# Kernel optimization log

Hardware: AMD Instinct MI355X
Metric: run time of the kernel (lower is better)

## Reference

```python
import jax, jax.numpy as jnp
import numpy as np

EPS_NORM = 1e-12  # torch F.normalize eps
EPS_POOL = 1e-06
GAMMA = 10.0
TOPK = 32


def _l2norm(x, axis):
    n = jnp.sqrt(jnp.sum(x * x, axis=axis, keepdims=True))
    return x / jnp.maximum(n, EPS_NORM)


def _sae(x, enc, dec_w, dec_b):
    # x: [N, D]; enc: [H, D]; dec_w: [D, H]; dec_b: [D]
    w = _l2norm(enc, axis=1)
    x_n = _l2norm(x, axis=-1)
    cos = jnp.clip(x_n @ w.T, -1.0, 1.0)           # [N, H]
    acts = 2.0 - jnp.sqrt(2.0 - 2.0 * cos)
    vals, idx = jax.lax.top_k(acts, TOPK)           # [N, K]
    rows = jnp.arange(acts.shape[0])[:, None]
    sparse = jnp.zeros_like(acts).at[rows, idx].set(vals)
    recon = sparse @ dec_w.T + dec_b                # [N, D]
    return recon, sparse


def _sample_views(v_pad, centers, H, W):
    # v_pad: [B, Lmax, D], centers: [B, K, 2]; uniform grid HxW per batch
    L = H * W
    y = (jnp.arange(H, dtype=jnp.float32) + 0.5) / H
    x = (jnp.arange(W, dtype=jnp.float32) + 0.5) / W
    gy, gx = jnp.meshgrid(y, x, indexing='ij')
    coords = jnp.stack([gx.ravel(), gy.ravel()], axis=-1)        # [L, 2] (x, y)
    diff = centers[:, :, None, :] - coords[None, None, :, :]     # [B, K, L, 2]
    m = jnp.exp(-GAMMA * jnp.sum(diff * diff, axis=-1))          # [B, K, L]
    num = jnp.einsum('bkl,bld->bkd', m, v_pad[:, :L, :])
    den = jnp.sum(m, axis=-1, keepdims=True) + EPS_POOL
    return num / den                                             # [B, K, D]


def setup_inputs() -> dict:
    key = jax.random.key(0)
    ks = jax.random.split(key, 10)
    B, Lmax, D, Hh, T, K = 64, 1024, 1024, 16384, 512, 8
    fan_in = D
    bound = 1.0 / np.sqrt(fan_in)
    return {
        'v_pad': jax.random.normal(ks[0], (B, Lmax, D), jnp.float32),
        'v_len': jnp.full((B,), Lmax, dtype=jnp.int32),
        'grid_thws': jnp.tile(jnp.array([[1, 32, 32]], dtype=jnp.int32), (B, 1)),
        't_pad': jax.random.normal(ks[1], (B, T, D), jnp.float32),
        't_mask': jnp.ones((B, T), jnp.float32),
        'centers': jax.random.uniform(ks[2], (B, K, 2), jnp.float32),
        'enc_v': jax.random.normal(ks[3], (Hh, D), jnp.float32) * 0.02,
        'dec_v_w': jax.random.uniform(ks[4], (D, Hh), jnp.float32, -bound, bound),
        'dec_v_b': jnp.zeros((D,), jnp.float32),
        'enc_t': jax.random.normal(ks[5], (Hh, D), jnp.float32) * 0.02,
        'dec_t_w': jax.random.uniform(ks[6], (D, Hh), jnp.float32, -bound, bound),
        'dec_t_b': jnp.zeros((D,), jnp.float32),
    }


def reference(v_pad, v_len, grid_thws, t_pad, t_mask, centers,
              enc_v, dec_v_w, dec_v_b, enc_t, dec_t_w, dec_t_b):
    H = int(np.asarray(grid_thws)[0, 1])
    W = int(np.asarray(grid_thws)[0, 2])
    # text global pooling
    t_sum = jnp.sum(t_pad * t_mask[..., None], axis=1)
    t_global = t_sum / (jnp.sum(t_mask, axis=1, keepdims=True) + EPS_POOL)
    # gaussian view pooling
    v_views = _sample_views(v_pad, centers, H, W)                 # [B, K, D]
    recon_t, latent_t = _sae(t_global, enc_t, dec_t_w, dec_t_b)
    B, K, D = v_views.shape
    recon_v_flat, latent_v_flat = _sae(v_views.reshape(B * K, D), enc_v, dec_v_w, dec_v_b)
    recon_v = recon_v_flat.reshape(B, K, D)
    latent_v = latent_v_flat.reshape(B, K, -1)
    return (recon_v, v_views, recon_t, t_global, latent_v, latent_t)
```

## Files before the change

### kernel.cpp

```cpp
#include <hip/hip_runtime.h>
#include <hip/hip_bf16.h>

constexpr int NB    = 64;
constexpr int LMAX  = 1024;
constexpr int DD    = 1024;
constexpr int HSAE  = 16384;
constexpr int TT    = 512;
constexpr int KV    = 8;
constexpr int TOPK  = 32;
constexpr int NROW_V = NB * KV;
constexpr int NROW_T = NB;

constexpr size_t OUT_RECON_V = 0;
constexpr size_t OUT_VVIEWS  = OUT_RECON_V + (size_t)NROW_V * DD;
constexpr size_t OUT_RECON_T = OUT_VVIEWS + (size_t)NROW_V * DD;
constexpr size_t OUT_TGLOBAL = OUT_RECON_T + (size_t)NROW_T * DD;
constexpr size_t OUT_LAT_V   = OUT_TGLOBAL + (size_t)NROW_T * DD;
constexpr size_t OUT_LAT_T   = OUT_LAT_V + (size_t)NROW_V * HSAE;

constexpr size_t WS_VN     = 0;
constexpr size_t WS_TN     = WS_VN + (size_t)NROW_V * DD;
constexpr size_t WS_IDX_V  = WS_TN + (size_t)NROW_T * DD;
constexpr size_t WS_VAL_V  = WS_IDX_V + (size_t)NROW_V * TOPK;
constexpr size_t WS_IDX_T  = WS_VAL_V + (size_t)NROW_V * TOPK;
constexpr size_t WS_VAL_T  = WS_IDX_T + (size_t)NROW_T * TOPK;
constexpr size_t WS_BINV_V = WS_VAL_T + (size_t)NROW_T * TOPK;
constexpr size_t WS_BINV_T = WS_BINV_V + (size_t)HSAE;
constexpr size_t WS_AHI_V  = WS_BINV_T + (size_t)HSAE;
constexpr size_t WS_AHI_T  = WS_AHI_V + (size_t)NROW_V * DD / 2;

constexpr int LC  = 8;
constexpr int LCH = LMAX / LC;
constexpr int TC  = 8;
constexpr int TCH = TT / TC;
constexpr size_t PV_NUM = 0;
constexpr size_t PV_DEN = (size_t)NB * LC * KV * DD;
constexpr size_t PT_NUM = 0;
constexpr size_t PT_DEN = (size_t)NB * TC * DD;

typedef __attribute__((ext_vector_type(8))) short bf16x8;
typedef __attribute__((ext_vector_type(4))) short s16x4;
typedef __attribute__((ext_vector_type(4))) float f32x4;

__device__ inline unsigned short f2bf_rn(float x) {
    unsigned u = __float_as_uint(x);
    return (unsigned short)((u + 0x7FFFu + ((u >> 16) & 1u)) >> 16);
}
__device__ inline double shfl_down_dbl(double x, int off) {
    long long l = __double_as_longlong(x);
    int lo = (int)(l & 0xffffffffll), hi = (int)(l >> 32);
    lo = __shfl_down(lo, off); hi = __shfl_down(hi, off);
    return __longlong_as_double(((long long)hi << 32) | (unsigned long long)(unsigned int)lo);
}

__global__ __launch_bounds__(256) void pool_part_kernel(const float* __restrict__ v_pad,
                                                        const float* __restrict__ centers,
                                                        const int* __restrict__ grid_thws,
                                                        const float* __restrict__ t_pad,
                                                        const float* __restrict__ t_mask,
                                                        float* __restrict__ partV,
                                                        float* __restrict__ partT) {
    __shared__ float m_s[LCH * KV];
    const int b   = blockIdx.x;
    const int tid = threadIdx.x;

    if (blockIdx.y < LC) {
        const int lc = blockIdx.y;
        const int H = grid_thws[1];
        const int W = grid_thws[2];
        int L = H * W; if (L > LMAX) L = LMAX;
        const int l0 = lc * LCH;

        for (int i = tid; i < LCH * KV; i += 256) {
            const int ll = i >> 3, k = i & 7;
            const int l  = l0 + ll;
            float m = 0.f;
            if (l < L) {
                const int iy = l / W, ix = l - iy * W;
                const float gx = (ix + 0.5f) / (float)W;
                const float gy = (iy + 0.5f) / (float)H;
                const float dx = centers[((size_t)b * KV + k) * 2 + 0] - gx;
                const float dy = centers[((size_t)b * KV + k) * 2 + 1] - gy;
                m = expf(-10.f * (dx * dx + dy * dy));
            }
            m_s[ll * KV + k] = m;
        }
        __syncthreads();
        if (tid < KV) {
            float s = 0.f;
            for (int ll = 0; ll < LCH; ++ll) s += m_s[ll * KV + tid];
            partV[PV_DEN + ((size_t)b * LC + lc) * KV + tid] = s;
        }

        const float* vp = v_pad + ((size_t)b * LMAX + l0) * DD + tid * 4;
        float4 acc[KV];
#pragma unroll
        for (int k = 0; k < KV; ++k) acc[k] = make_float4(0.f, 0.f, 0.f, 0.f);
#pragma unroll 4
        for (int ll = 0; ll < LCH; ++ll) {
            const float4 v = *(const float4*)(vp + (size_t)ll * DD);
#pragma unroll
            for (int k = 0; k < KV; ++k) {
                const float m = m_s[ll * KV + k];
                acc[k].x = fmaf(m, v.x, acc[k].x); acc[k].y = fmaf(m, v.y, acc[k].y);
                acc[k].z = fmaf(m, v.z, acc[k].z); acc[k].w = fmaf(m, v.w, acc[k].w);
            }
        }
#pragma unroll
        for (int k = 0; k < KV; ++k)
            *(float4*)(partV + PV_NUM + (((size_t)b * LC + lc) * KV + k) * DD + tid * 4) = acc[k];
    } else {
        const int tc = blockIdx.y - LC;
        const int t0 = tc * TCH;
        if (tid < TCH) m_s[tid] = t_mask[(size_t)b * TT + t0 + tid];
        __syncthreads();
        if (tid == 0) {
            float s = 0.f;
            for (int i = 0; i < TCH; ++i) s += m_s[i];
            partT[PT_DEN + (size_t)b * TC + tc] = s;
        }
        const float* tp = t_pad + ((size_t)b * TT + t0) * DD + tid * 4;
        float4 acc = make_float4(0.f, 0.f, 0.f, 0.f);
#pragma unroll 4
        for (int t = 0; t < TCH; ++t) {
            const float4 v = *(const float4*)(tp + (size_t)t * DD);
            const float m = m_s[t];
            acc.x = fmaf(m, v.x, acc.x); acc.y = fmaf(m, v.y, acc.y);
            acc.z = fmaf(m, v.z, acc.z); acc.w = fmaf(m, v.w, acc.w);
        }
        *(float4*)(partT + PT_NUM + ((size_t)b * TC + tc) * DD + tid * 4) = acc;
    }
}

__device__ inline void comb_norm_emit(float4 vv, int r, int tid,
                                      float* __restrict__ out_row,
                                      float* __restrict__ ws, size_t xn_off, size_t hi_off) {
    *(float4*)(out_row + tid * 4) = vv;
    float ss = vv.x * vv.x + vv.y * vv.y + vv.z * vv.z + vv.w * vv.w;
#pragma unroll
    for (int off = 32; off; off >>= 1) ss += __shfl_down(ss, off);
    __shared__ float wsum[4];
    if ((tid & 63) == 0) wsum[tid >> 6] = ss;
    __syncthreads();
    const float tot = wsum[0] + wsum[1] + wsum[2] + wsum[3];
    const float scale = 1.f / fmaxf(sqrtf(tot), 1e-12f);
    float4 xn;
    xn.x = vv.x * scale; xn.y = vv.y * scale; xn.z = vv.z * scale; xn.w = vv.w * scale;
    *(float4*)(ws + xn_off + (size_t)r * DD + tid * 4) = xn;
    const float f[4] = {xn.x, xn.y, xn.z, xn.w};
    s16x4 hv;
#pragma unroll
    for (int c = 0; c < 4; ++c) hv[c] = (short)f2bf_rn(f[c]);
    *(s16x4*)((short*)(ws + hi_off) + (size_t)r * DD + tid * 4) = hv;
}

__global__ __launch_bounds__(256) void pool_comb_kernel(const float* __restrict__ partV,
                                                        const float* __restrict__ partT,
                                                        float* __restrict__ out_views,
                                                        float* __restrict__ out_tg,
                                                        float* __restrict__ ws) {
    const int b   = blockIdx.x;
    const int k   = blockIdx.y;
    const int tid = threadIdx.x;
    if (k < KV) {
        float den = 1e-6f;
        for (int lc = 0; lc < LC; ++lc) den += partV[PV_DEN + ((size_t)b * LC + lc) * KV + k];
        float4 s = make_float4(0.f, 0.f, 0.f, 0.f);
        for (int lc = 0; lc < LC; ++lc) {
            const float4 p = *(const float4*)(partV + PV_NUM + (((size_t)b * LC + lc) * KV + k) * DD + tid * 4);
            s.x += p.x; s.y += p.y; s.z += p.z; s.w += p.w;
        }
        const float inv = 1.f / den;
        float4 vv = make_float4(s.x * inv, s.y * inv, s.z * inv, s.w * inv);
        const int r = b * KV + k;
        comb_norm_emit(vv, r, tid, out_views + (size_t)r * DD, ws, WS_VN, WS_AHI_V);
    } else {
        float den = 1e-6f;
        for (int tc = 0; tc < TC; ++tc) den += partT[PT_DEN + (size_t)b * TC + tc];
        float4 s = make_float4(0.f, 0.f, 0.f, 0.f);
        for (int tc = 0; tc < TC; ++tc) {
            const float4 p = *(const float4*)(partT + PT_NUM + ((size_t)b * TC + tc) * DD + tid * 4);
            s.x += p.x; s.y += p.y; s.z += p.z; s.w += p.w;
        }
        const float inv = 1.f / den;
        float4 vv = make_float4(s.x * inv, s.y * inv, s.z * inv, s.w * inv);
        comb_norm_emit(vv, b, tid, out_tg + (size_t)b * DD, ws, WS_TN, WS_AHI_T);
    }
}

constexpr int GBM = 128, GBN = 64, GBK = 32;

__device__ inline int fragoff(int sub, int g, int r16) {
    return (((sub * 4 + g) * 16) + (r16 ^ ((g & 3) << 1))) * 8;
}

__global__ __launch_bounds__(256) void gemm_acts_mfma(const float* __restrict__ encV,
                                                      const float* __restrict__ encT,
                                                      float* __restrict__ out,
                                                      float* __restrict__ ws) {
    __shared__ short Ah[GBM * GBK];
    __shared__ short Bh[GBN * GBK], Bl[GBN * GBK];
    __shared__ float bn_part[GBN][4];
    __shared__ float binv_s[GBN];

    const int tid  = threadIdx.x;
    const int lane = tid & 63;
    const int wv   = tid >> 6;
    const int wm   = wv & 1;
    const int wn   = wv >> 1;
    const int bid  = blockIdx.x;
    const int xcd  = bid & 7;
    const int slot = bid >> 3;
    const int hb   = xcd + 8 * (slot / 5);
    const int my   = slot % 5;
    const bool isT = (my == 4);
    const int h0   = hb * GBN;
    const int m0   = isT ? 0 : my * GBM;
    const int M    = isT ? NROW_T : NROW_V;
    const float* Bm = isT ? encT : encV;
    const short* AhiP = (const short*)(ws + (isT ? WS_AHI_T : WS_AHI_V));
    float* outActs = out + (isT ? OUT_LAT_T : OUT_LAT_V);
    float* binv_g  = ws + (isT ? WS_BINV_T : WS_BINV_V);

    const int ksS = tid & 3;
    int lrA[2];
#pragma unroll
    for (int rt = 0; rt < 2; ++rt) lrA[rt] = (rt * 256 + tid) >> 2;
    const int lrB = tid >> 2;

    f32x4 acc[4][2];
#pragma unroll
    for (int mi = 0; mi < 4; ++mi)
#pragma unroll
        for (int ni = 0; ni < 2; ++ni) acc[mi][ni] = (f32x4){0.f, 0.f, 0.f, 0.f};
    float bnacc = 0.f;

    bf16x8 pa[2];
    float4 pb0, pb1;

    auto issue_loads = [&](int kt) {
#pragma unroll
        for (int rt = 0; rt < 2; ++rt) {
            if (m0 + lrA[rt] < M)
                pa[rt] = *(const bf16x8*)&AhiP[(size_t)(m0 + lrA[rt]) * DD + kt + ksS * 8];
            else
                pa[rt] = (bf16x8){0, 0, 0, 0, 0, 0, 0, 0};
        }
        const float* src = Bm + (size_t)(h0 + lrB) * DD + kt + ksS * 8;
        pb0 = *(const float4*)src;
        pb1 = *(const float4*)(src + 4);
    };

    auto write_lds = [&]() {
#pragma unroll
        for (int rt = 0; rt < 2; ++rt)
            *(bf16x8*)&Ah[fragoff(lrA[rt] >> 4, ksS, lrA[rt] & 15)] = pa[rt];
        {
            const float f[8] = {pb0.x, pb0.y, pb0.z, pb0.w, pb1.x, pb1.y, pb1.z, pb1.w};
            bf16x8 hv, lv;
            float bsum = 0.f;
#pragma unroll
            for (int j = 0; j < 8; ++j) {
                const unsigned short hb16 = f2bf_rn(f[j]);
                const float hf = __uint_as_float((unsigned)hb16 << 16);
                hv[j] = (short)hb16;
                lv[j] = (short)f2bf_rn(f[j] - hf);
                bsum = fmaf(f[j], f[j], bsum);
            }
            bnacc += bsum;
            const int off = fragoff(lrB >> 4, ksS, lrB & 15);
            *(bf16x8*)&Bh[off] = hv; *(bf16x8*)&Bl[off] = lv;
        }
    };

    issue_loads(0);
    for (int kt = 0; kt < DD; kt += GBK) {
        write_lds();
        __syncthreads();
        if (kt + GBK < DD) issue_loads(kt + GBK);

        {
            bf16x8 ah[4], bh[2], bl[2];
            const int g = lane >> 4;
            const int r16 = lane & 15;
#pragma unroll
            for (int t = 0; t < 4; ++t)
                ah[t] = *(const bf16x8*)&Ah[fragoff(wm * 4 + t, g, r16)];
#pragma unroll
            for (int t = 0; t < 2; ++t) {
                const int bo = fragoff(wn * 2 + t, g, r16);
                bh[t] = *(const bf16x8*)&Bh[bo];
                bl[t] = *(const bf16x8*)&Bl[bo];
            }
#pragma unroll
            for (int mi = 0; mi < 4; ++mi)
#pragma unroll
                for (int ni = 0; ni < 2; ++ni) {
                    acc[mi][ni] = __builtin_amdgcn_mfma_f32_16x16x32_bf16(ah[mi], bh[ni], acc[mi][ni], 0, 0, 0);
                    acc[mi][ni] = __builtin_amdgcn_mfma_f32_16x16x32_bf16(ah[mi], bl[ni], acc[mi][ni], 0, 0, 0);
                }
        }
        __syncthreads();
    }

    bn_part[lrB][ksS] = bnacc;
    __syncthreads();
    if (tid < GBN) {
        float s = bn_part[tid][0] + bn_part[tid][1] + bn_part[tid][2] + bn_part[tid][3];
        const float bi = 1.f / fmaxf(sqrtf(s), 1e-12f);
        binv_s[tid] = bi;
        if (my == 0 || my == 4) binv_g[h0 + tid] = bi;
    }
    __syncthreads();

#pragma unroll
    for (int mi = 0; mi < 4; ++mi)
#pragma unroll
        for (int ni = 0; ni < 2; ++ni) {
            const int hl = wn * 32 + ni * 16 + (lane & 15);
            const float bi = binv_s[hl];
#pragma unroll
            for (int j = 0; j < 4; ++j) {
                const int m = m0 + wm * 64 + mi * 16 + (lane >> 4) * 4 + j;
                if (m < M) {
                    float c = acc[mi][ni][j] * bi;
                    c = fminf(1.f, fmaxf(-1.f, c));
                    outActs[(size_t)m * HSAE + h0 + hl] = 2.f - sqrtf(fmaxf(0.f, 2.f - 2.f * c));
                }
            }
        }
}

constexpr int NBINS = 2048;
constexpr int NFINE = 256;
constexpr int CAP   = 512;
constexpr int BANDCAP = 128;
constexpr int MARGIN  = 12;
constexpr float RANKEPS = 2.5e-4f;

__global__ __launch_bounds__(256) void topk_kernel(float* __restrict__ out_buf,
                                                   float* __restrict__ ws,
                                                   const float* __restrict__ enc_v,
                                                   const float* __restrict__ enc_t) {
    const int r    = blockIdx.x;
    const int tid  = threadIdx.x;
    const int wv   = tid >> 6;
    const int lane = tid & 63;
    float* row;
    int* idxp; float* valp;
    const float* xn; const float* enc; const float* binv;
    if (r < NROW_V) {
        row  = out_buf + OUT_LAT_V + (size_t)r * HSAE;
        idxp = (int*)(ws + WS_IDX_V) + (size_t)r * TOPK;
        valp = ws + WS_VAL_V + (size_t)r * TOPK;
        xn   = ws + WS_VN + (size_t)r * DD;
        enc  = enc_v; binv = ws + WS_BINV_V;
    } else {
        const int rr = r - NROW_V;
        row  = out_buf + OUT_LAT_T + (size_t)rr * HSAE;
        idxp = (int*)(ws + WS_IDX_T) + (size_t)rr * TOPK;
        valp = ws + WS_VAL_T + (size_t)rr * TOPK;
        xn   = ws + WS_TN + (size_t)rr * DD;
        enc  = enc_t; binv = ws + WS_BINV_T;
    }

    __shared__ unsigned int hist[4][NBINS];
    __shared__ unsigned int fine[4][NFINE];
    __shared__ float xs[DD];
    __shared__ unsigned long long cand[CAP];
    __shared__ unsigned long long ord[CAP];
    __shared__ double bval[BANDCAP];
    __shared__ int    bidx[BANDCAP];
    __shared__ int s_ncand, s_bin, s_cntgt, s_sub, s_A, s_E;

    for (int i = tid; i < 4 * NBINS; i += 256) ((unsigned int*)hist)[i] = 0u;
    for (int i = tid; i < 4 * NFINE; i += 256) ((unsigned int*)fine)[i] = 0u;
    if (tid == 0) { s_ncand = 0; }
    *(float4*)&xs[tid * 4] = *(const float4*)&xn[tid * 4];

    unsigned int bcache[64];
#pragma unroll
    for (int e = 0; e < 16; ++e) {
        const float4 v = *(const float4*)(row + (size_t)e * 1024 + tid * 4);
        bcache[e * 4 + 0] = __float_as_uint(v.x);
        bcache[e * 4 + 1] = __float_as_uint(v.y);
        bcache[e * 4 + 2] = __float_as_uint(v.z);
        bcache[e * 4 + 3] = __float_as_uint(v.w);
    }
#pragma unroll
    for (int e = 0; e < 16; ++e)
        *(float4*)(row + (size_t)e * 1024 + tid * 4) = make_float4(0.f, 0.f, 0.f, 0.f);
    __syncthreads();

#pragma unroll
    for (int e = 0; e < 64; ++e) {
        unsigned int bin = bcache[e] >> 19;
        if (bin > NBINS - 1) bin = NBINS - 1;
        atomicAdd(&hist[wv][bin], 1u);
    }
    __syncthreads();
    for (int i = tid; i < NBINS; i += 256)
        hist[0][i] += hist[1][i] + hist[2][i] + hist[3][i];
    __syncthreads();

    if (tid < 64) {
        unsigned int csum = 0;
#pragma unroll
        for (int j = 0; j < 32; ++j)
            csum += hist[0][tid * 32 + ((tid + j) & 31)];
        unsigned int suf = csum;
#pragma unroll
        for (int off = 1; off < 64; off <<= 1) {
            unsigned int o = __shfl_down(suf, off);
            suf += (tid + off < 64) ? o : 0u;
        }
        if (suf >= (unsigned)TOPK && (suf - csum) < (unsigned)TOPK) {
            unsigned int run = suf - csum;
            int b = tid * 32 + 31;
            for (; b > tid * 32; --b) {
                const unsigned int h = hist[0][b];
                if (run + h >= (unsigned)TOPK) break;
                run += h;
            }
            s_bin = b; s_cntgt = (int)run;
        }
    }
    __syncthreads();
    const unsigned int B0 = (unsigned int)s_bin;
    const int r0 = TOPK - s_cntgt;

#pragma unroll
    for (int e = 0; e < 64; ++e) {
        const unsigned int bits = bcache[e];
        unsigned int bin = bits >> 19;
        if (bin > NBINS - 1) bin = NBINS - 1;
        if (bin == B0) atomicAdd(&fine[wv][(bits >> 11) & 255u], 1u);
    }
    __syncthreads();
    for (int i = tid; i < NFINE; i += 256)
        fine[0][i] += fine[1][i] + fine[2][i] + fine[3][i];
    __syncthreads();

    if (tid < 64) {
        unsigned int csum = fine[0][tid * 4] + fine[0][tid * 4 + 1] +
                            fine[0][tid * 4 + 2] + fine[0][tid * 4 + 3];
        unsigned int suf = csum;
#pragma unroll
        for (int off = 1; off < 64; off <<= 1) {
            unsigned int o = __shfl_down(suf, off);
            suf += (tid + off < 64) ? o : 0u;
        }
        if (suf >= (unsigned)r0 && (suf - csum) < (unsigned)r0) {
            unsigned int run = suf - csum;
            int b = tid * 4 + 3;
            for (; b > tid * 4; --b) {
                const unsigned int h = fine[0][b];
                if (run + h >= (unsigned)r0) break;
                run += h;
            }
            s_sub = b;
        }
    }
    __syncthreads();
    const unsigned int cf0 = (B0 << 8) | (unsigned)s_sub;
    const unsigned int cfTh = cf0 - (unsigned)MARGIN;

#pragma unroll
    for (int e = 0; e < 64; ++e) {
        const unsigned int bits = bcache[e];
        if ((bits >> 11) >= cfTh) {
            const int slot = atomicAdd(&s_ncand, 1);
            if (slot < CAP) {
                const unsigned int idx = (unsigned)(e >> 2) * 1024u + (unsigned)tid * 4u + (unsigned)(e & 3);
                cand[slot] = ((unsigned long long)bits << 32) | (unsigned long long)(16383u - idx);
            }
        }
    }
    __syncthreads();
    const int nc = (s_ncand < CAP) ? s_ncand : CAP;

    for (int i = tid; i < nc; i += 256) {
        const unsigned long long K = cand[i];
        int rank = 0;
        for (int j = 0; j < nc; ++j) rank += (cand[j] > K) ? 1 : 0;
        ord[rank] = K;
    }
    if (tid == 0) { s_A = nc; s_E = nc; }
    __syncthreads();

    const float Tv = __uint_as_float((unsigned)(ord[31] >> 32));
    for (int i = tid; i < nc; i += 256) {
        const float v = __uint_as_float((unsigned)(ord[i] >> 32));
        if (v <= Tv + 2.f * RANKEPS) atomicMin(&s_A, i);
        if (v <  Tv - 2.f * RANKEPS) atomicMin(&s_E, i);
    }
    __syncthreads();
    const int A = s_A;
    int E = s_E; if (E > A + BANDCAP) E = A + BANDCAP;
    const int nb = E - A;

    for (int t = A + wv; t < E; t += 4) {
        const int idx = 16383 - (int)(ord[t] & 0xffffffffull);
        const float* er = enc + (size_t)idx * DD;
        double s = 0.0;
#pragma unroll
        for (int i = 0; i < 16; ++i) {
            const int j = lane + i * 64;
            s = fma((double)xs[j], (double)er[j], s);
        }
#pragma unroll
        for (int off = 32; off; off >>= 1) s += shfl_down_dbl(s, off);
        if (lane == 0) {
            double c = s * (double)binv[idx];
            c = fmin(1.0, fmax(-1.0, c));
            bval[t - A] = 2.0 - sqrt(fmax(0.0, 2.0 - 2.0 * c));
            bidx[t - A] = idx;
        }
    }
    __syncthreads();

    for (int i = tid; i < A; i += 256) {
        const int idx  = 16383 - (int)(ord[i] & 0xffffffffull);
        const float v  = __uint_as_float((unsigned)(ord[i] >> 32));
        idxp[i] = idx; valp[i] = v; row[idx] = v;
    }
    for (int t = tid; t < nb; t += 256) {
        int fr = 0;
        for (int u = 0; u < nb; ++u)
            if (bval[u] > bval[t] || (bval[u] == bval[t] && bidx[u] < bidx[t])) fr++;
        const int slot = A + fr;
        if (slot < TOPK) {
            const float v = (float)bval[t];
            idxp[slot] = bidx[t]; valp[slot] = v; row[bidx[t]] = v;
        }
    }
}

__global__ __launch_bounds__(256) void recon_kernel(const float* __restrict__ dvw,
                                                    const float* __restrict__ dvb,
                                                    const float* __restrict__ dtw,
                                                    const float* __restrict__ dtb,
                                                    const float* __restrict__ ws,
                                                    float* __restrict__ out) {
    __shared__ float wrow[HSAE];
    const int bid = blockIdx.x;
    const bool isT = bid >= DD;
    const int d   = isT ? bid - DD : bid;
    const int tid = threadIdx.x;
    const float* decw = isT ? dtw : dvw;
    const float* decb = isT ? dtb : dvb;
    const int*   idxp = (const int*)(ws + (isT ? WS_IDX_T : WS_IDX_V));
    const float* valp = ws + (isT ? WS_VAL_T : WS_VAL_V);
    float* outp = out + (isT ? OUT_RECON_T : OUT_RECON_V);
    const int M = isT ? NROW_T : NROW_V;

    const float* wr = decw + (size_t)d * HSAE;
    for (int e = 0; e < HSAE / (256 * 4); ++e)
        *(float4*)&wrow[(size_t)(e * 256 + tid) * 4] = *(const float4*)(wr + (size_t)(e * 256 + tid) * 4);
    __syncthreads();
    const float bias = decb[d];
    for (int n = tid; n < M; n += 256) {
        float acc = bias;
#pragma unroll
        for (int k = 0; k < TOPK; ++k)
            acc = fmaf(valp[n * TOPK + k], wrow[idxp[n * TOPK + k]], acc);
        outp[(size_t)n * DD + d] = acc;
    }
}

extern "C" void kernel_launch(void* const* d_in, const int* in_sizes, int n_in,
                              void* d_out, int out_size, void* d_ws, size_t ws_size,
                              hipStream_t stream) {
    const float* v_pad    = (const float*)d_in[0];
    const int*   grid_thws = (const int*)d_in[2];
    const float* t_pad    = (const float*)d_in[3];
    const float* t_mask   = (const float*)d_in[4];
    const float* centers  = (const float*)d_in[5];
    const float* enc_v    = (const float*)d_in[6];
    const float* dec_v_w  = (const float*)d_in[7];
    const float* dec_v_b  = (const float*)d_in[8];
    const float* enc_t    = (const float*)d_in[9];
    const float* dec_t_w  = (const float*)d_in[10];
    const float* dec_t_b  = (const float*)d_in[11];
    float* out = (float*)d_out;
    float* ws  = (float*)d_ws;

    pool_part_kernel<<<dim3(NB, LC + TC), 256, 0, stream>>>(v_pad, centers, grid_thws, t_pad, t_mask,
                                                            out + OUT_LAT_V, out + OUT_LAT_T);
    pool_comb_kernel<<<dim3(NB, KV + 1), 256, 0, stream>>>(out + OUT_LAT_V, out + OUT_LAT_T,
                                                           out + OUT_VVIEWS, out + OUT_TGLOBAL, ws);
    gemm_acts_mfma<<<1280, 256, 0, stream>>>(enc_v, enc_t, out, ws);
    topk_kernel<<<NROW_V + NROW_T, 256, 0, stream>>>(out, ws, enc_v, enc_t);
    recon_kernel<<<2 * DD, 256, 0, stream>>>(dec_v_w, dec_v_b, dec_t_w, dec_t_b, ws, out);
}
```

Before: 264.3 us.

## Drop bf16 lo-part split for encoder weights and shrink GEMM M tile

Encoder weights are now rounded to a single bf16 value instead of a hi+lo split, which halves the MFMA count and removes the Bl LDS buffer. The M tile also shrinks from 128 to 64, so each block does less work and the grid grows from 1280 to 2304 blocks. This trades cosine accuracy for less compute. Lower precision can change which entries top-k selects near ties, and the smaller tile loads each weight tile more times.

```diff
diff --git a/kernel.cpp b/kernel.cpp
--- a/kernel.cpp
+++ b/kernel.cpp
@@ -188,7 +188,8 @@
     }
 }
 
-constexpr int GBM = 128, GBN = 64, GBK = 32;
+constexpr int GBM = 64, GBN = 64, GBK = 32;
+constexpr int MY_SLOTS = NROW_V / GBM + 1;
 
 __device__ inline int fragoff(int sub, int g, int r16) {
     return (((sub * 4 + g) * 16) + (r16 ^ ((g & 3) << 1))) * 8;
@@ -199,7 +200,7 @@
                                                       float* __restrict__ out,
                                                       float* __restrict__ ws) {
     __shared__ short Ah[GBM * GBK];
-    __shared__ short Bh[GBN * GBK], Bl[GBN * GBK];
+    __shared__ short Bh[GBN * GBK];
     __shared__ float bn_part[GBN][4];
     __shared__ float binv_s[GBN];
 
@@ -211,9 +212,9 @@
     const int bid  = blockIdx.x;
     const int xcd  = bid & 7;
     const int slot = bid >> 3;
-    const int hb   = xcd + 8 * (slot / 5);
-    const int my   = slot % 5;
-    const bool isT = (my == 4);
+    const int hb   = xcd + 8 * (slot / MY_SLOTS);
+    const int my   = slot % MY_SLOTS;
+    const bool isT = (my == MY_SLOTS - 1);
     const int h0   = hb * GBN;
     const int m0   = isT ? 0 : my * GBM;
     const int M    = isT ? NROW_T : NROW_V;
@@ -223,53 +224,42 @@
     float* binv_g  = ws + (isT ? WS_BINV_T : WS_BINV_V);
 
     const int ksS = tid & 3;
-    int lrA[2];
-#pragma unroll
-    for (int rt = 0; rt < 2; ++rt) lrA[rt] = (rt * 256 + tid) >> 2;
+    const int lrA = tid >> 2;
     const int lrB = tid >> 2;
 
-    f32x4 acc[4][2];
-#pragma unroll
-    for (int mi = 0; mi < 4; ++mi)
+    f32x4 acc[2][2];
+#pragma unroll
+    for (int mi = 0; mi < 2; ++mi)
 #pragma unroll
         for (int ni = 0; ni < 2; ++ni) acc[mi][ni] = (f32x4){0.f, 0.f, 0.f, 0.f};
     float bnacc = 0.f;
 
-    bf16x8 pa[2];
+    bf16x8 pa;
     float4 pb0, pb1;
 
     auto issue_loads = [&](int kt) {
-#pragma unroll
-        for (int rt = 0; rt < 2; ++rt) {
-            if (m0 + lrA[rt] < M)
-                pa[rt] = *(const bf16x8*)&AhiP[(size_t)(m0 + lrA[rt]) * DD + kt + ksS * 8];
-            else
-                pa[rt] = (bf16x8){0, 0, 0, 0, 0, 0, 0, 0};
-        }
+        if (m0 + lrA < M)
+            pa = *(const bf16x8*)&AhiP[(size_t)(m0 + lrA) * DD + kt + ksS * 8];
+        else
+            pa = (bf16x8){0, 0, 0, 0, 0, 0, 0, 0};
         const float* src = Bm + (size_t)(h0 + lrB) * DD + kt + ksS * 8;
         pb0 = *(const float4*)src;
         pb1 = *(const float4*)(src + 4);
     };
 
     auto write_lds = [&]() {
-#pragma unroll
-        for (int rt = 0; rt < 2; ++rt)
-            *(bf16x8*)&Ah[fragoff(lrA[rt] >> 4, ksS, lrA[rt] & 15)] = pa[rt];
+        *(bf16x8*)&Ah[fragoff(lrA >> 4, ksS, lrA & 15)] = pa;
         {
             const float f[8] = {pb0.x, pb0.y, pb0.z, pb0.w, pb1.x, pb1.y, pb1.z, pb1.w};
-            bf16x8 hv, lv;
+            bf16x8 hv;
             float bsum = 0.f;
 #pragma unroll
             for (int j = 0; j < 8; ++j) {
-                const unsigned short hb16 = f2bf_rn(f[j]);
-                const float hf = __uint_as_float((unsigned)hb16 << 16);
-                hv[j] = (short)hb16;
-                lv[j] = (short)f2bf_rn(f[j] - hf);
+                hv[j] = (short)f2bf_rn(f[j]);
                 bsum = fmaf(f[j], f[j], bsum);
             }
             bnacc += bsum;
-            const int off = fragoff(lrB >> 4, ksS, lrB & 15);
-            *(bf16x8*)&Bh[off] = hv; *(bf16x8*)&Bl[off] = lv;
+            *(bf16x8*)&Bh[fragoff(lrB >> 4, ksS, lrB & 15)] = hv;
         }
     };
 
@@ -280,25 +270,19 @@
         if (kt + GBK < DD) issue_loads(kt + GBK);
 
         {
-            bf16x8 ah[4], bh[2], bl[2];
+            bf16x8 ah[2], bh[2];
             const int g = lane >> 4;
             const int r16 = lane & 15;
 #pragma unroll
-            for (int t = 0; t < 4; ++t)
-                ah[t] = *(const bf16x8*)&Ah[fragoff(wm * 4 + t, g, r16)];
-#pragma unroll
             for (int t = 0; t < 2; ++t) {
-                const int bo = fragoff(wn * 2 + t, g, r16);
-                bh[t] = *(const bf16x8*)&Bh[bo];
-                bl[t] = *(const bf16x8*)&Bl[bo];
-            }
-#pragma unroll
-            for (int mi = 0; mi < 4; ++mi)
-#pragma unroll
-                for (int ni = 0; ni < 2; ++ni) {
+                ah[t] = *(const bf16x8*)&Ah[fragoff(wm * 2 + t, g, r16)];
+                bh[t] = *(const bf16x8*)&Bh[fragoff(wn * 2 + t, g, r16)];
+            }
+#pragma unroll
+            for (int mi = 0; mi < 2; ++mi)
+#pragma unroll
+                for (int ni = 0; ni < 2; ++ni)
                     acc[mi][ni] = __builtin_amdgcn_mfma_f32_16x16x32_bf16(ah[mi], bh[ni], acc[mi][ni], 0, 0, 0);
-                    acc[mi][ni] = __builtin_amdgcn_mfma_f32_16x16x32_bf16(ah[mi], bl[ni], acc[mi][ni], 0, 0, 0);
-                }
         }
         __syncthreads();
     }
@@ -309,19 +293,19 @@
         float s = bn_part[tid][0] + bn_part[tid][1] + bn_part[tid][2] + bn_part[tid][3];
         const float bi = 1.f / fmaxf(sqrtf(s), 1e-12f);
         binv_s[tid] = bi;
-        if (my == 0 || my == 4) binv_g[h0 + tid] = bi;
-    }
-    __syncthreads();
-
-#pragma unroll
-    for (int mi = 0; mi < 4; ++mi)
+        if (my == 0 || isT) binv_g[h0 + tid] = bi;
+    }
+    __syncthreads();
+
+#pragma unroll
+    for (int mi = 0; mi < 2; ++mi)
 #pragma unroll
         for (int ni = 0; ni < 2; ++ni) {
             const int hl = wn * 32 + ni * 16 + (lane & 15);
             const float bi = binv_s[hl];
 #pragma unroll
             for (int j = 0; j < 4; ++j) {
-                const int m = m0 + wm * 64 + mi * 16 + (lane >> 4) * 4 + j;
+                const int m = m0 + wm * 32 + mi * 16 + (lane >> 4) * 4 + j;
                 if (m < M) {
                     float c = acc[mi][ni][j] * bi;
                     c = fminf(1.f, fmaxf(-1.f, c));
@@ -589,7 +573,7 @@
                                                             out + OUT_LAT_V, out + OUT_LAT_T);
     pool_comb_kernel<<<dim3(NB, KV + 1), 256, 0, stream>>>(out + OUT_LAT_V, out + OUT_LAT_T,
                                                            out + OUT_VVIEWS, out + OUT_TGLOBAL, ws);
-    gemm_acts_mfma<<<1280, 256, 0, stream>>>(enc_v, enc_t, out, ws);
+    gemm_acts_mfma<<<(HSAE / GBN) * MY_SLOTS * 1, 256, 0, stream>>>(enc_v, enc_t, out, ws);
     topk_kernel<<<NROW_V + NROW_T, 256, 0, stream>>>(out, ws, enc_v, enc_t);
     recon_kernel<<<2 * DD, 256, 0, stream>>>(dec_v_w, dec_v_b, dec_t_w, dec_t_b, ws, out);
 }
```

After: 267.3 us. Within noise of the previous version (+1.1%).

## Double GEMM M-tile to 256 rows to cut redundant encoder-weight loads

Applied to the files above, without the earlier changes.

The acts GEMM block tile grows from 128 to 256 rows, so each block computes two 128-row sub-tiles per K step against the same B tile. Each encoder column tile is then loaded and split into bf16 hi/lo fewer times, which cuts global fp32 reads of the encoder weights and the conversion work. The price is a smaller grid (768 blocks instead of 1280), twice the accumulator registers, and a text slot whose block covers only 64 of its 256 rows, leaving that work imbalanced. There is also a leftover no-op condition in the B fragment offset.

```diff
diff --git a/kernel.cpp b/kernel.cpp
--- a/kernel.cpp
+++ b/kernel.cpp
@@ -188,7 +188,8 @@
     }
 }
 
-constexpr int GBM = 128, GBN = 64, GBK = 32;
+constexpr int GBM = 256, GBN = 64, GBK = 32;
+constexpr int MY_SLOTS = NROW_V / GBM + 1;
 
 __device__ inline int fragoff(int sub, int g, int r16) {
     return (((sub * 4 + g) * 16) + (r16 ^ ((g & 3) << 1))) * 8;
@@ -211,9 +212,9 @@
     const int bid  = blockIdx.x;
     const int xcd  = bid & 7;
     const int slot = bid >> 3;
-    const int hb   = xcd + 8 * (slot / 5);
-    const int my   = slot % 5;
-    const bool isT = (my == 4);
+    const int hb   = xcd + 8 * (slot / MY_SLOTS);
+    const int my   = slot % MY_SLOTS;
+    const bool isT = (my == MY_SLOTS - 1);
     const int h0   = hb * GBN;
     const int m0   = isT ? 0 : my * GBM;
     const int M    = isT ? NROW_T : NROW_V;
@@ -223,24 +224,26 @@
     float* binv_g  = ws + (isT ? WS_BINV_T : WS_BINV_V);
 
     const int ksS = tid & 3;
-    int lrA[2];
-#pragma unroll
-    for (int rt = 0; rt < 2; ++rt) lrA[rt] = (rt * 256 + tid) >> 2;
+    int lrA[4];
+#pragma unroll
+    for (int rt = 0; rt < 4; ++rt) lrA[rt] = (rt * 256 + tid) >> 2;
     const int lrB = tid >> 2;
 
-    f32x4 acc[4][2];
-#pragma unroll
-    for (int mi = 0; mi < 4; ++mi)
-#pragma unroll
-        for (int ni = 0; ni < 2; ++ni) acc[mi][ni] = (f32x4){0.f, 0.f, 0.f, 0.f};
+    f32x4 acc[2][4][2];
+#pragma unroll
+    for (int mt = 0; mt < 2; ++mt)
+#pragma unroll
+        for (int mi = 0; mi < 4; ++mi)
+#pragma unroll
+            for (int ni = 0; ni < 2; ++ni) acc[mt][mi][ni] = (f32x4){0.f, 0.f, 0.f, 0.f};
     float bnacc = 0.f;
 
-    bf16x8 pa[2];
+    bf16x8 pa[4];
     float4 pb0, pb1;
 
     auto issue_loads = [&](int kt) {
 #pragma unroll
-        for (int rt = 0; rt < 2; ++rt) {
+        for (int rt = 0; rt < 4; ++rt) {
             if (m0 + lrA[rt] < M)
                 pa[rt] = *(const bf16x8*)&AhiP[(size_t)(m0 + lrA[rt]) * DD + kt + ksS * 8];
             else
@@ -253,7 +256,7 @@
 
     auto write_lds = [&]() {
 #pragma unroll
-        for (int rt = 0; rt < 2; ++rt)
+        for (int rt = 0; rt < 4; ++rt)
             *(bf16x8*)&Ah[fragoff(lrA[rt] >> 4, ksS, lrA[rt] & 15)] = pa[rt];
         {
             const float f[8] = {pb0.x, pb0.y, pb0.z, pb0.w, pb1.x, pb1.y, pb1.z, pb1.w};
@@ -280,25 +283,29 @@
         if (kt + GBK < DD) issue_loads(kt + GBK);
 
         {
-            bf16x8 ah[4], bh[2], bl[2];
+            bf16x8 bh[2], bl[2];
             const int g = lane >> 4;
             const int r16 = lane & 15;
 #pragma unroll
-            for (int t = 0; t < 4; ++t)
-                ah[t] = *(const bf16x8*)&Ah[fragoff(wm * 4 + t, g, r16)];
-#pragma unroll
             for (int t = 0; t < 2; ++t) {
-                const int bo = fragoff(wn * 2 + t, g, r16);
+                const int bo = fragoff(lrB >= 0 ? (wn * 2 + t) : 0, g, r16);
                 bh[t] = *(const bf16x8*)&Bh[bo];
                 bl[t] = *(const bf16x8*)&Bl[bo];
             }
 #pragma unroll
-            for (int mi = 0; mi < 4; ++mi)
-#pragma unroll
-                for (int ni = 0; ni < 2; ++ni) {
-                    acc[mi][ni] = __builtin_amdgcn_mfma_f32_16x16x32_bf16(ah[mi], bh[ni], acc[mi][ni], 0, 0, 0);
-                    acc[mi][ni] = __builtin_amdgcn_mfma_f32_16x16x32_bf16(ah[mi], bl[ni], acc[mi][ni], 0, 0, 0);
-                }
+            for (int mt = 0; mt < 2; ++mt) {
+                bf16x8 ah[4];
+#pragma unroll
+                for (int t = 0; t < 4; ++t)
+                    ah[t] = *(const bf16x8*)&Ah[fragoff(mt * 8 + wm * 4 + t, g, r16)];
+#pragma unroll
+                for (int mi = 0; mi < 4; ++mi)
+#pragma unroll
+                    for (int ni = 0; ni < 2; ++ni) {
+                        acc[mt][mi][ni] = __builtin_amdgcn_mfma_f32_16x16x32_bf16(ah[mi], bh[ni], acc[mt][mi][ni], 0, 0, 0);
+                        acc[mt][mi][ni] = __builtin_amdgcn_mfma_f32_16x16x32_bf16(ah[mi], bl[ni], acc[mt][mi][ni], 0, 0, 0);
+                    }
+            }
         }
         __syncthreads();
     }
@@ -309,26 +316,28 @@
         float s = bn_part[tid][0] + bn_part[tid][1] + bn_part[tid][2] + bn_part[tid][3];
         const float bi = 1.f / fmaxf(sqrtf(s), 1e-12f);
         binv_s[tid] = bi;
-        if (my == 0 || my == 4) binv_g[h0 + tid] = bi;
-    }
-    __syncthreads();
-
-#pragma unroll
-    for (int mi = 0; mi < 4; ++mi)
-#pragma unroll
-        for (int ni = 0; ni < 2; ++ni) {
-            const int hl = wn * 32 + ni * 16 + (lane & 15);
-            const float bi = binv_s[hl];
-#pragma unroll
-            for (int j = 0; j < 4; ++j) {
-                const int m = m0 + wm * 64 + mi * 16 + (lane >> 4) * 4 + j;
-                if (m < M) {
-                    float c = acc[mi][ni][j] * bi;
-                    c = fminf(1.f, fmaxf(-1.f, c));
-                    outActs[(size_t)m * HSAE + h0 + hl] = 2.f - sqrtf(fmaxf(0.f, 2.f - 2.f * c));
+        if (my == 0 || isT) binv_g[h0 + tid] = bi;
+    }
+    __syncthreads();
+
+#pragma unroll
+    for (int mt = 0; mt < 2; ++mt)
+#pragma unroll
+        for (int mi = 0; mi < 4; ++mi)
+#pragma unroll
+            for (int ni = 0; ni < 2; ++ni) {
+                const int hl = wn * 32 + ni * 16 + (lane & 15);
+                const float bi = binv_s[hl];
+#pragma unroll
+                for (int j = 0; j < 4; ++j) {
+                    const int m = m0 + mt * 128 + wm * 64 + mi * 16 + (lane >> 4) * 4 + j;
+                    if (m < M) {
+                        float c = acc[mt][mi][ni][j] * bi;
+                        c = fminf(1.f, fmaxf(-1.f, c));
+                        outActs[(size_t)m * HSAE + h0 + hl] = 2.f - sqrtf(fmaxf(0.f, 2.f - 2.f * c));
+                    }
                 }
             }
-        }
 }
 
 constexpr int NBINS = 2048;
@@ -589,7 +598,7 @@
                                                             out + OUT_LAT_V, out + OUT_LAT_T);
     pool_comb_kernel<<<dim3(NB, KV + 1), 256, 0, stream>>>(out + OUT_LAT_V, out + OUT_LAT_T,
                                                            out + OUT_VVIEWS, out + OUT_TGLOBAL, ws);
-    gemm_acts_mfma<<<1280, 256, 0, stream>>>(enc_v, enc_t, out, ws);
+    gemm_acts_mfma<<<(HSAE / GBN) * MY_SLOTS, 256, 0, stream>>>(enc_v, enc_t, out, ws);
     topk_kernel<<<NROW_V + NROW_T, 256, 0, stream>>>(out, ws, enc_v, enc_t);
     recon_kernel<<<2 * DD, 256, 0, stream>>>(dec_v_w, dec_v_b, dec_t_w, dec_t_b, ws, out);
 }
```

Measured after the change: 272.0 us. 1.03x slower.
